# Performance work log

Hardware: AMD Instinct MI355X
Metric: run time of the kernel (lower is better)

## Reference

```python
import jax, jax.numpy as jnp
import numpy as np
from jax import lax

BASE_SIZE = 16.0
FEAT_STRIDE = 16
RATIOS = (0.5, 1.0, 2.0)
SCALES = (8.0, 16.0, 32.0)
N_PRE_NMS = 6000   # eval-mode ProposalCreator defaults
N_POST_NMS = 300
NMS_THRESH = 0.7
MIN_SIZE = 16.0
SCALE = 1.0


def anchor_base():
    # generate_anchor_base: loops ratio-major, scale-minor -> 9 anchors (y1,x1,y2,x2)
    r = jnp.asarray(RATIOS, jnp.float32)
    s = jnp.asarray(SCALES, jnp.float32)
    h = (BASE_SIZE * s[None, :] * jnp.sqrt(r)[:, None]).reshape(-1)
    w = (BASE_SIZE * s[None, :] * jnp.sqrt(1.0 / r)[:, None]).reshape(-1)
    c = BASE_SIZE / 2.0
    return jnp.stack([c - h / 2, c - w / 2, c + h / 2, c + w / 2], axis=1)  # [9,4]


def enumerate_anchors(hh, ww):
    # replicates _enumerate_shift_anchor incl. torch.meshgrid(shift_x, shift_y) 'ij' ordering
    sy = jnp.arange(hh, dtype=jnp.float32) * FEAT_STRIDE
    sx = jnp.arange(ww, dtype=jnp.float32) * FEAT_STRIDE
    gx, gy = jnp.meshgrid(sx, sy, indexing='ij')  # shapes [ww, hh]
    shift = jnp.stack([gy.ravel(), gx.ravel(), gy.ravel(), gx.ravel()], axis=1)  # [K,4]
    a = anchor_base()[None, :, :] + shift[:, None, :]  # [K,9,4]
    return a.reshape(-1, 4)


def conv2d(x, w, b, pad):
    y = lax.conv_general_dilated(x, w, (1, 1), [(pad, pad), (pad, pad)],
                                 dimension_numbers=('NCHW', 'OIHW', 'NCHW'))
    return y + b[None, :, None, None]


def loc2bbox(anchor, loc):
    h = anchor[:, 2] - anchor[:, 0]
    w = anchor[:, 3] - anchor[:, 1]
    cy = anchor[:, 0] + 0.5 * h
    cx = anchor[:, 1] + 0.5 * w
    dy, dx, dh, dw = loc[:, 0], loc[:, 1], loc[:, 2], loc[:, 3]
    cy = dy * h + cy
    cx = dx * w + cx
    h = jnp.exp(dh) * h
    w = jnp.exp(dw) * w
    return jnp.stack([cy - 0.5 * h, cx - 0.5 * w, cy + 0.5 * h, cx + 0.5 * w], axis=1)


def propose(loc, score, anchor, img_h, img_w):
    # ProposalCreator for a single image: decode, clip, min-size filter, top-k, NMS, pad to N_POST_NMS
    roi = loc2bbox(anchor, loc)
    roi = jnp.stack([jnp.clip(roi[:, 0], 0.0, img_h), jnp.clip(roi[:, 1], 0.0, img_w),
                     jnp.clip(roi[:, 2], 0.0, img_h), jnp.clip(roi[:, 3], 0.0, img_w)], axis=1)
    ms = MIN_SIZE * SCALE
    valid = ((roi[:, 2] - roi[:, 0]) >= ms) & ((roi[:, 3] - roi[:, 1]) >= ms)
    score = jnp.where(valid, score, -jnp.inf)
    top_s, order = lax.top_k(score, N_PRE_NMS)          # score-descending candidates
    boxes = roi[order]                                   # [N_PRE,4]
    valid_s = top_s > -jnp.inf
    # pairwise IoU [N_PRE,N_PRE]
    area = (boxes[:, 2] - boxes[:, 0]) * (boxes[:, 3] - boxes[:, 1])
    tl = jnp.maximum(boxes[:, None, :2], boxes[None, :, :2])
    br = jnp.minimum(boxes[:, None, 2:], boxes[None, :, 2:])
    inter = jnp.prod(jnp.clip(br - tl, 0.0, None), axis=-1)
    iou = lax.stop_gradient(inter / (area[:, None] + area[None, :] - inter))
    idxs = jnp.arange(N_PRE_NMS)
    def body(keep, i):
        sup = (iou[i] > NMS_THRESH) & (idxs > i) & keep[i]
        return keep & ~sup, None
    keep, _ = lax.scan(body, valid_s, idxs)              # greedy NMS over score-sorted boxes
    # kept indices in score order (stable argsort: True(kept) sorts first as 0)
    sel = jnp.argsort(jnp.logical_not(keep))[:N_POST_NMS]
    out_valid = jnp.arange(N_POST_NMS) < jnp.sum(keep)
    return jnp.where(out_valid[:, None], boxes[sel], 0.0)  # [N_POST,4], zero-padded


def rpn_forward(x, conv1_w, conv1_b, score_w, score_b, loc_w, loc_b, img_h, img_w):
    n, _, hh, ww = x.shape
    anchor = enumerate_anchors(hh, ww)                   # [hh*ww*9, 4]
    A = anchor.shape[0] // (hh * ww)
    feat = jax.nn.relu(conv2d(x, conv1_w, conv1_b, 1))   # [n,512,hh,ww]
    locs = conv2d(feat, loc_w, loc_b, 0).transpose(0, 2, 3, 1).reshape(n, -1, 4)
    raw_scores = conv2d(feat, score_w, score_b, 0).transpose(0, 2, 3, 1)  # [n,hh,ww,A*2]
    fg = jax.nn.softmax(raw_scores.reshape(n, hh, ww, A, 2), axis=4)[..., 1].reshape(n, -1)
    scores = raw_scores.reshape(n, -1, 2)
    rois = jax.vmap(lambda l, s: propose(l, s, anchor, float(img_h), float(img_w)))(locs, fg)
    roi_indices = jnp.broadcast_to(jnp.arange(n, dtype=jnp.int32)[:, None], (n, N_POST_NMS))
    return locs, scores, rois, roi_indices, anchor


def setup_inputs() -> dict:
    key = jax.random.key(0)
    ks = jax.random.split(key, 4)
    x = jax.random.normal(ks[0], (4, 512, 50, 50), jnp.float32)
    conv1_w = jax.random.normal(ks[1], (512, 512, 3, 3), jnp.float32) * 0.01
    conv1_b = jnp.zeros((512,), jnp.float32)
    score_w = jax.random.normal(ks[2], (18, 512, 1, 1), jnp.float32) * 0.01
    score_b = jnp.zeros((18,), jnp.float32)
    loc_w = jax.random.normal(ks[3], (36, 512, 1, 1), jnp.float32) * 0.01
    loc_b = jnp.zeros((36,), jnp.float32)
    return {'x': x, 'conv1_w': conv1_w, 'conv1_b': conv1_b, 'score_w': score_w,
            'score_b': score_b, 'loc_w': loc_w, 'loc_b': loc_b, 'img_h': 800, 'img_w': 800}


def reference(x, conv1_w, conv1_b, score_w, score_b, loc_w, loc_b, img_h, img_w):
    return rpn_forward(x, conv1_w, conv1_b, score_w, score_b, loc_w, loc_b, img_h, img_w)
```

## Files before the change

kernel.cpp:

```cpp
#include <hip/hip_runtime.h>
#include <stdint.h>

#define NB 4
#define CIN 512
#define PIX 2500
#define KTOT 4608
#define NBOX 22500
#define NPRE 6000
#define NPOST 300
#define NWORD 94
#define SCAP 8192

#define O_LOCS   0
#define O_SCORES 360000
#define O_ROIS   540000
#define O_RIDX   544800
#define O_ANCH   546000

#define XT_ROWS 2960
#define XT_FRONT 64
#define XT_IMG (XT_ROWS * 512)
#define XT_SPLIT_BYTES ((size_t)NB * XT_IMG * 2)

#define WO_XT1   0ull
#define WO_XT2   12124160ull
#define WO_WSBLK 24248320ull
#define WO_FEATP 33685504ull
#define WO_WT    74645504ull
#define WO_BOXES 74760192ull
#define WO_DKEY  76200192ull
#define WO_BOX6K 76560192ull
#define WO_VALID 76944192ull
#define WO_MASK  0ull

#define FEATP_HALF 5120000

typedef _Float16 h8 __attribute__((ext_vector_type(8)));
typedef float f32x4 __attribute__((ext_vector_type(4)));
typedef unsigned int u32;
typedef unsigned long long u64;

__device__ __forceinline__ void gll16(const void* g, void* l) {
  __builtin_amdgcn_global_load_lds((const __attribute__((address_space(1))) u32*)g,
                                   (__attribute__((address_space(3))) u32*)l, 16, 0, 0);
}

__device__ __forceinline__ float rd_dim(const int* p) {
  int v = *p;
  if (v > 0 && v < 1000000) return (float)v;
  return __int_as_float(v);
}

__global__ void k_zero(u32* __restrict__ xt) {
  size_t n = (2 * XT_SPLIT_BYTES) / 4;
  for (size_t i = blockIdx.x * 256ull + threadIdx.x; i < n; i += (size_t)gridDim.x * 256)
    xt[i] = 0u;
}

__global__ void k_xT(const float* __restrict__ x, _Float16* __restrict__ x1,
                     _Float16* __restrict__ x2) {
  __shared__ float sx[3200];
  int chunk = blockIdx.x, r0 = blockIdx.y, b = blockIdx.z;
  int t = threadIdx.x;
  int ic0 = chunk * 64;
  for (int i = t; i < 3200; i += 256) {
    int icl = i / 50, c = i - icl * 50;
    sx[i] = x[(((size_t)b * 512 + ic0 + icl) * 50 + r0) * 50 + c];
  }
  __syncthreads();
  for (int j = t; j < 3200; j += 256) {
    int c = j >> 6, icl = j & 63;
    float v = sx[icl * 50 + c];
    _Float16 h1 = (_Float16)v;
    _Float16 h2 = (_Float16)(v - (float)h1);
    size_t dst = (size_t)b * XT_IMG + (size_t)(XT_FRONT + (r0 + 1) * 52 + (c + 1)) * 512 + ic0 + icl;
    x1[dst] = h1;
    x2[dst] = h2;
  }
}

__global__ void k_splitw(const float* __restrict__ w, _Float16* __restrict__ wblk) {
  int n = 4 * 144 * 16 * 512;
  for (int idx = blockIdx.x * 256 + threadIdx.x; idx < n; idx += gridDim.x * 256) {
    int lane8 = idx & 511;
    int l = lane8 >> 3, j = lane8 & 7;
    int reg = (idx >> 9) & 15;
    int t = idx >> 13;
    int ksI = t % 144, mt = t / 144;
    int ocs = reg >> 1, s = reg & 1;
    int oc = mt * 128 + ocs * 16 + (l & 15);
    int k = ksI * 32 + (l >> 4) * 8 + j;
    int tap = k >> 9, ic = k & 511;
    float v = w[((size_t)oc * 512 + ic) * 9 + tap];
    _Float16 h1 = (_Float16)v;
    wblk[idx] = s ? (_Float16)(v - (float)h1) : h1;
  }
}

__global__ void k_wt(const float* __restrict__ loc_w, const float* __restrict__ score_w,
                     float* __restrict__ wt) {
  int idx = blockIdx.x * 256 + threadIdx.x;
  if (idx >= 128 * 56 * 4) return;
  int i = idx & 3, j = (idx >> 2) % 56, c4 = idx / 224;
  int c = c4 * 4 + i;
  float v = 0.f;
  if (j < 36) v = loc_w[(size_t)j * 512 + c];
  else if (j < 54) v = score_w[(size_t)(j - 36) * 512 + c];
  wt[idx] = v;
}

__global__ __launch_bounds__(128, 2) void k_conv(
    const _Float16* __restrict__ xs1, const _Float16* __restrict__ xs2,
    const _Float16* __restrict__ wsBlk,
    float* __restrict__ featP) {
  __shared__ _Float16 lds[16384];
  int id = blockIdx.x;
  int bz = id & 7;
  int inner = id >> 3;
  int st = inner / 44;
  int idx2 = inner - st * 44;
  int nt = idx2 >> 1;
  int mt = st * 2 + (idx2 & 1);
  int b = bz >> 1, ks = bz & 1;
  int t = threadIdx.x, lane = t & 63, w = t >> 6;
  int mb = mt * 128, nb = nt * 128;
  int l15 = lane & 15, l4 = lane >> 4;
  const _Float16* xi1 = xs1 + (size_t)b * XT_IMG + (size_t)XT_FRONT * 512;
  const _Float16* xi2 = xs2 + (size_t)b * XT_IMG + (size_t)XT_FRONT * 512;
  const _Float16* wbase = wsBlk + ((size_t)(mt * 144 + ks * 72) * 16 + w * 8) * 512 + lane * 8;

  f32x4 acc[4][8];
#pragma unroll
  for (int i = 0; i < 4; i++)
#pragma unroll
    for (int j = 0; j < 8; j++)
      acc[i][j] = (f32x4){0.f, 0.f, 0.f, 0.f};

  auto stageB = [&](int kk, int off) {
    int kg = ks * 2304 + kk * 32;
    int tap = kg >> 9, ic0 = kg & 511;
    int sh = (tap / 3 - 1) * 52 + (tap % 3) - 1;
#pragma unroll
    for (int u = 0; u < 8; u++) {
      int r = w * 8 + u;
      int pxs = r >> 1, s = r & 1;
      const _Float16* xp = s ? xi2 : xi1;
      int qp = nb + pxs * 16 + l15 + sh;
      gll16(xp + (ptrdiff_t)qp * 512 + ic0 + l4 * 8, &lds[off + r * 512]);
    }
  };
  auto loadA = [&](int kk, h8* a) {
    const _Float16* p = wbase + (size_t)kk * 16 * 512;
#pragma unroll
    for (int u = 0; u < 8; u++) a[u] = *(const h8*)(p + u * 512);
  };
  auto compute = [&](int off, const h8* a) {
#pragma unroll
    for (int nf = 0; nf < 8; nf++) {
      h8 b0 = *(const h8*)&lds[off + (nf * 2 + 0) * 512 + lane * 8];
      h8 b1 = *(const h8*)&lds[off + (nf * 2 + 1) * 512 + lane * 8];
      __builtin_amdgcn_s_setprio(1);
#pragma unroll
      for (int mf = 0; mf < 4; mf++) {
        acc[mf][nf] = __builtin_amdgcn_mfma_f32_16x16x32_f16(a[mf * 2 + 0], b0, acc[mf][nf], 0, 0, 0);
        acc[mf][nf] = __builtin_amdgcn_mfma_f32_16x16x32_f16(a[mf * 2 + 0], b1, acc[mf][nf], 0, 0, 0);
        acc[mf][nf] = __builtin_amdgcn_mfma_f32_16x16x32_f16(a[mf * 2 + 1], b0, acc[mf][nf], 0, 0, 0);
      }
      __builtin_amdgcn_s_setprio(0);
    }
  };

  h8 aA[8], aB[8];
  loadA(0, aA);
  stageB(0, 0);
  __syncthreads();
#pragma unroll 1
  for (int kp = 0; kp < 36; kp++) {
    int kk = 2 * kp;
    stageB(kk + 1, 8192);
    loadA(kk + 1, aB);
    compute(0, aA);
    __syncthreads();
    if (kp < 35) {
      stageB(kk + 2, 0);
      loadA(kk + 2, aA);
    }
    compute(8192, aB);
    __syncthreads();
  }

  float* fp = featP + (size_t)ks * FEATP_HALF;
#pragma unroll
  for (int nf = 0; nf < 8; nf++) {
    int q = nb + nf * 16 + l15;
    int r = q / 52, c = q - r * 52;
    if (r >= 1 && r <= 50 && c >= 1 && c <= 50) {
      int p = (r - 1) * 50 + (c - 1);
      size_t base = ((size_t)b * PIX + p) * 512;
#pragma unroll
      for (int mf = 0; mf < 4; mf++) {
        int oc0 = mb + w * 64 + mf * 16 + l4 * 4;
        *(float4*)&fp[base + oc0] = make_float4(acc[mf][nf][0], acc[mf][nf][1],
                                                acc[mf][nf][2], acc[mf][nf][3]);
      }
    }
  }
}

__global__ __launch_bounds__(256) void k_heads(const float* __restrict__ featP,
                                               const float* __restrict__ wt4,
                                               const float* __restrict__ conv_b,
                                               const float* __restrict__ loc_b,
                                               const float* __restrict__ score_b,
                                               const int* __restrict__ ihp,
                                               const int* __restrict__ iwp,
                                               float* __restrict__ out,
                                               float* __restrict__ boxes,
                                               uint32_t* __restrict__ dkey) {
  int wid = blockIdx.x * 4 + (threadIdx.x >> 6);
  if (wid >= NB * PIX) return;
  int lane = threadIdx.x & 63;
  int b = wid / PIX, p = wid % PIX;
  int row = lane < 54 ? lane : 54;
  const float* f0 = featP + ((size_t)b * PIX + p) * 512;
  const float* f1 = f0 + FEATP_HALF;
  float acc = 0.f;
  for (int c4 = 0; c4 < 128; c4++) {
    float4 u = *(const float4*)(f0 + c4 * 4);
    float4 v = *(const float4*)(f1 + c4 * 4);
    float4 bb = *(const float4*)(conv_b + c4 * 4);
    float4 wv = *(const float4*)(wt4 + ((size_t)c4 * 56 + row) * 4);
    acc += fmaxf(u.x + v.x + bb.x, 0.f) * wv.x;
    acc += fmaxf(u.y + v.y + bb.y, 0.f) * wv.y;
    acc += fmaxf(u.z + v.z + bb.z, 0.f) * wv.z;
    acc += fmaxf(u.w + v.w + bb.w, 0.f) * wv.w;
  }
  float bi = 0.f;
  if (lane < 36) bi = loc_b[lane];
  else if (lane < 54) bi = score_b[lane - 36];
  acc += bi;
  if (lane < 36) out[O_LOCS + (size_t)b * 90000 + (size_t)p * 36 + lane] = acc;
  else if (lane < 54) out[O_SCORES + (size_t)b * 45000 + (size_t)p * 18 + (lane - 36)] = acc;

  float imgH = rd_dim(ihp), imgW = rd_dim(iwp);
  int gy = p % 50, gx = p / 50;
  float sy = 16.f * gy, sx = 16.f * gx;

  int a9 = (lane < 9) ? lane : 0;
  float dy  = __shfl(acc, a9 * 4 + 0);
  float dxv = __shfl(acc, a9 * 4 + 1);
  float dh  = __shfl(acc, a9 * 4 + 2);
  float dw  = __shfl(acc, a9 * 4 + 3);
  float l0  = __shfl(acc, 36 + a9 * 2);
  float l1  = __shfl(acc, 36 + a9 * 2 + 1);

  {
    float rr = (a9 < 3) ? 0.5f : (a9 < 6 ? 1.f : 2.f);
    int si = a9 % 3;
    float ssc = (si == 0) ? 8.f : (si == 1 ? 16.f : 32.f);
    float hb = 16.f * ssc * sqrtf(rr);
    float wb = 16.f * ssc * sqrtf(1.f / rr);
    float ay1 = (8.f - hb * 0.5f) + sy;
    float ax1 = (8.f - wb * 0.5f) + sx;
    float ay2 = (8.f + hb * 0.5f) + sy;
    float ax2 = (8.f + wb * 0.5f) + sx;
    float h = ay2 - ay1, w2d = ax2 - ax1;
    float cy = ay1 + 0.5f * h, cx = ax1 + 0.5f * w2d;
    float cy2 = dy * h + cy, cx2 = dxv * w2d + cx;
    float h2 = expf(dh) * h, ww2 = expf(dw) * w2d;
    float y1 = cy2 - 0.5f * h2, x1 = cx2 - 0.5f * ww2;
    float y2 = cy2 + 0.5f * h2, x2 = cx2 + 0.5f * ww2;
    y1 = fminf(fmaxf(y1, 0.f), imgH);
    x1 = fminf(fmaxf(x1, 0.f), imgW);
    y2 = fminf(fmaxf(y2, 0.f), imgH);
    x2 = fminf(fmaxf(x2, 0.f), imgW);
    bool valid = (y2 - y1 >= 16.f) && (x2 - x1 >= 16.f);
    float m = fmaxf(l0, l1);
    float e0 = expf(l0 - m), e1 = expf(l1 - m);
    float fg = e1 / (e0 + e1);
    float scv = valid ? fg : -INFINITY;
    if (lane < 9) {
      size_t k = (size_t)b * NBOX + (size_t)p * 9 + a9;
      *(float4*)(boxes + k * 4) = make_float4(y1, x1, y2, x2);
      uint32_t u = __float_as_uint(scv);
      uint32_t f2 = (u >> 31) ? ~u : (u | 0x80000000u);
      dkey[k] = ~f2;
    }
  }
  if (b == 0 && lane < 36) {
    int aa = lane >> 2, dd = lane & 3;
    float rr2 = (aa < 3) ? 0.5f : (aa < 6 ? 1.f : 2.f);
    int si2 = aa % 3;
    float ss2 = (si2 == 0) ? 8.f : (si2 == 1 ? 16.f : 32.f);
    float hb2 = 16.f * ss2 * sqrtf(rr2);
    float wb2 = 16.f * ss2 * sqrtf(1.f / rr2);
    float v;
    if (dd == 0) v = (8.f - hb2 * 0.5f) + sy;
    else if (dd == 1) v = (8.f - wb2 * 0.5f) + sx;
    else if (dd == 2) v = (8.f + hb2 * 0.5f) + sy;
    else v = (8.f + wb2 * 0.5f) + sx;
    out[O_ANCH + (size_t)p * 36 + lane] = v;
  }
}

__global__ void k_topk(const uint32_t* __restrict__ dkey, const float* __restrict__ boxes,
                       float* __restrict__ box6k,
                       unsigned long long* __restrict__ validm) {
  extern __shared__ char smem[];
  u64* cand = (u64*)smem;
  u64* alt  = (u64*)(smem + 65536);
  u32* hcnt = (u32*)(smem + 131072);
  u32* wc     = (u32*)(smem + 139264);
  u32* digTot = wc + 16;
  u32* digBase = digTot + 16;
  u32* msc = digBase + 16;
  u32* histw = (u32*)(smem + 65536);
  u32* hist = histw + 4096;
  int b = blockIdx.x, tid = threadIdx.x;
  int wq = tid >> 6, l = tid & 63;
  const uint32_t* dk = dkey + (size_t)b * NBOX;

  uint32_t P = 0, need = NPRE;
  for (int pass = 0; pass < 4; pass++) {
    int sh = 24 - 8 * pass;
    for (int i = tid; i < 16 * 256; i += 1024) histw[i] = 0;
    __syncthreads();
    for (int i = tid; i < NBOX; i += 1024) {
      uint32_t d = dk[i];
      bool match = (((uint64_t)d >> (sh + 8)) == ((uint64_t)P >> (sh + 8)));
      if (match) atomicAdd(&histw[wq * 256 + ((d >> sh) & 255u)], 1u);
    }
    __syncthreads();
    for (int bin = tid; bin < 256; bin += 1024) {
      uint32_t s = 0;
#pragma unroll
      for (int q = 0; q < 16; q++) s += histw[q * 256 + bin];
      hist[bin] = s;
    }
    __syncthreads();
    if (tid == 0) {
      uint32_t cum = 0, v = 0;
      for (; v < 255; v++) {
        if (cum + hist[v] >= need) break;
        cum += hist[v];
      }
      msc[0] = v;
      msc[1] = cum;
    }
    __syncthreads();
    need -= msc[1];
    P |= msc[0] << sh;
    __syncthreads();
  }
  uint32_t Dstar = P;

  if (tid == 0) msc[2] = 0;
  __syncthreads();
  for (int c = 0; c < 22; c++) {
    int i = c * 1024 + tid;
    uint32_t d = (i < NBOX) ? dk[i] : 0xFFFFFFFFu;
    bool pred = (i < NBOX) && (d <= Dstar);
    u64 bal = __ballot(pred);
    uint32_t rank = (uint32_t)__popcll(bal & ((1ull << l) - 1ull));
    __syncthreads();
    if (l == 0) wc[wq] = (uint32_t)__popcll(bal);
    __syncthreads();
    if (tid == 0) {
      uint32_t run = msc[2];
      for (int q = 0; q < 16; q++) { uint32_t v = wc[q]; wc[q] = run; run += v; }
      msc[2] = run;
    }
    __syncthreads();
    if (pred) {
      uint32_t pos = wc[wq] + rank;
      if (pos < SCAP) cand[pos] = ((u64)d << 32) | (uint32_t)i;
    }
  }
  __syncthreads();
  uint32_t cnt = msc[2] < SCAP ? msc[2] : SCAP;
  for (int i = (int)cnt + tid; i < SCAP; i += 1024) cand[i] = ~0ull;
  __syncthreads();

  u64* src = cand;
  u64* dst = alt;
  for (int pass = 0; pass < 8; pass++) {
    int sh = 32 + pass * 4;
    for (int i = tid; i < 2048; i += 1024) hcnt[i] = 0;
    __syncthreads();
    for (int c = 0; c < 8; c++) {
      int i = c * 1024 + tid;
      uint32_t dig = (uint32_t)(src[i] >> sh) & 15u;
      u64 m = ~0ull;
#pragma unroll
      for (int bit = 0; bit < 4; bit++) {
        u64 bb = __ballot((dig >> bit) & 1u);
        m &= ((dig >> bit) & 1u) ? bb : ~bb;
      }
      if (l == __builtin_ctzll(m)) hcnt[(i >> 6) * 16 + dig] = (uint32_t)__popcll(m);
    }
    __syncthreads();
    if (tid < 16) {
      uint32_t run = 0;
      for (int u = 0; u < 128; u++) {
        uint32_t v = hcnt[u * 16 + tid];
        hcnt[u * 16 + tid] = run;
        run += v;
      }
      digTot[tid] = run;
    }
    __syncthreads();
    if (tid == 0) {
      uint32_t basev = 0;
      for (int d2 = 0; d2 < 16; d2++) { digBase[d2] = basev; basev += digTot[d2]; }
    }
    __syncthreads();
    for (int c = 0; c < 8; c++) {
      int i = c * 1024 + tid;
      u64 key = src[i];
      uint32_t dig = (uint32_t)(key >> sh) & 15u;
      u64 m = ~0ull;
#pragma unroll
      for (int bit = 0; bit < 4; bit++) {
        u64 bb = __ballot((dig >> bit) & 1u);
        m &= ((dig >> bit) & 1u) ? bb : ~bb;
      }
      uint32_t rank = (uint32_t)__popcll(m & ((1ull << l) - 1ull));
      uint32_t dpos = digBase[dig] + hcnt[(i >> 6) * 16 + dig] + rank;
      dst[dpos] = key;
    }
    __syncthreads();
    u64* tmp = src; src = dst; dst = tmp;
  }

  for (int r = tid; r < NPRE; r += 1024) {
    u64 kk = cand[r];
    uint32_t idx = (uint32_t)kk;
    float4 bx = *(const float4*)(boxes + ((size_t)b * NBOX + idx) * 4);
    *(float4*)(box6k + ((size_t)b * NPRE + r) * 4) = bx;
  }
  for (int wi = tid; wi < NWORD; wi += 1024) {
    unsigned long long m = 0ull;
    for (int bb = 0; bb < 64; bb++) {
      int r = wi * 64 + bb;
      if (r < NPRE) {
        uint32_t d = (uint32_t)(cand[r] >> 32);
        if (d < 0xFF800000u) m |= (1ull << bb);
      }
    }
    validm[b * NWORD + wi] = m;
  }
}

__global__ __launch_bounds__(256) void k_mask(const float* __restrict__ box6k,
                                              unsigned long long* __restrict__ mask) {
  int b = blockIdx.z, it = blockIdx.x, wt = blockIdx.y;
  int t = threadIdx.x;
  int il = t & 31, wl = t >> 5;
  if (wt * 512 + 511 <= it * 32) return;
  __shared__ float bi[32][4];
  __shared__ float bj[512][4];
  if (t < 128) {
    int ii = it * 32 + (t >> 2);
    if (ii > NPRE - 1) ii = NPRE - 1;
    bi[t >> 2][t & 3] = box6k[((size_t)b * NPRE + ii) * 4 + (t & 3)];
  }
#pragma unroll
  for (int q = 0; q < 2; q++) {
    int v = t + 256 * q;
    int jg = wt * 512 + v;
    float4 f = make_float4(0.f, 0.f, 0.f, 0.f);
    if (jg < NPRE) f = *(const float4*)(box6k + ((size_t)b * NPRE + jg) * 4);
    *(float4*)&bj[v][0] = f;
  }
  __syncthreads();
  int i = it * 32 + il;
  int w = wt * 8 + wl;
  if (i >= NPRE || w >= NWORD) return;
  float y1 = bi[il][0], x1 = bi[il][1], y2 = bi[il][2], x2 = bi[il][3];
  float ar = (y2 - y1) * (x2 - x1);
  unsigned long long m = 0ull;
  int jbase = w * 64;
  for (int jj = 0; jj < 64; jj++) {
    int j = jbase + jj;
    int js = wl * 64 + jj;
    float jy1 = bj[js][0], jx1 = bj[js][1], jy2 = bj[js][2], jx2 = bj[js][3];
    float tlY = fmaxf(y1, jy1), tlX = fmaxf(x1, jx1);
    float brY = fminf(y2, jy2), brX = fminf(x2, jx2);
    float ih = fmaxf(brY - tlY, 0.f), iw2 = fmaxf(brX - tlX, 0.f);
    float inter = ih * iw2;
    float arj = (jy2 - jy1) * (jx2 - jx1);
    float iou = inter / (ar + arj - inter);
    if (iou > 0.7f && j > i && j < NPRE) m |= (1ull << jj);
  }
  mask[((size_t)b * NPRE + i) * NWORD + w] = m;
}

__global__ void k_scan(const unsigned long long* __restrict__ mask,
                       const unsigned long long* __restrict__ validm,
                       const float* __restrict__ box6k, float* __restrict__ out) {
  int b = blockIdx.x;
  int lane = threadIdx.x;
  const unsigned long long* mb = mask + (size_t)b * NPRE * NWORD;
  u64 a0 = (lane < NWORD) ? validm[b * NWORD + lane] : 0ull;
  u64 a1 = (lane + 64 < NWORD) ? validm[b * NWORD + lane + 64] : 0ull;
  __shared__ int keptIdx[NPOST];
  int cnt = 0;
  bool done = false;
  u64 rowCur = mb[(size_t)lane * NWORD + 0];
  for (int w = 0; w < NWORD && !done; w++) {
    u64 rowNext = 0ull;
    if (w + 1 < NWORD) {
      int i2 = (w + 1) * 64 + lane;
      if (i2 < NPRE) rowNext = mb[(size_t)i2 * NWORD + (w + 1)];
    }
    u64 alive = (w < 64) ? __shfl(a0, w) : __shfl(a1, w - 64);
    if (alive) {
      u64 keep = 0ull;
      while (alive) {
        int q = __builtin_ctzll(alive);
        alive &= alive - 1;
        keep |= (1ull << q);
        if (lane == 0) keptIdx[cnt] = w * 64 + q;
        cnt++;
        if (cnt >= NPOST) { done = true; break; }
        alive &= ~__shfl(rowCur, q);
      }
      if (w < 64) { if (lane == w) a0 = 0ull; }
      else        { if (lane == w - 64) a1 = 0ull; }
      if (!done) {
        while (keep) {
          u64 or0 = 0ull, or1 = 0ull;
#pragma unroll
          for (int z = 0; z < 8; z++) {
            if (keep) {
              int q = __builtin_ctzll(keep);
              keep &= keep - 1;
              int ki = w * 64 + q;
              u64 m0 = (lane < NWORD && lane > w) ? mb[(size_t)ki * NWORD + lane] : 0ull;
              u64 m1 = (lane + 64 < NWORD && lane + 64 > w) ? mb[(size_t)ki * NWORD + 64 + lane] : 0ull;
              or0 |= m0;
              or1 |= m1;
            }
          }
          a0 &= ~or0;
          a1 &= ~or1;
        }
      }
    }
    rowCur = rowNext;
  }
  __syncthreads();
  for (int r = lane; r < NPOST; r += 64) {
    float4 bx = make_float4(0.f, 0.f, 0.f, 0.f);
    if (r < cnt) bx = *(const float4*)(box6k + ((size_t)b * NPRE + keptIdx[r]) * 4);
    *(float4*)(out + O_ROIS + ((size_t)b * NPOST + r) * 4) = bx;
    out[O_RIDX + b * NPOST + r] = (float)b;
  }
}

extern "C" void kernel_launch(void* const* d_in, const int* in_sizes, int n_in,
                              void* d_out, int out_size, void* d_ws, size_t ws_size,
                              hipStream_t stream) {
  const float* x       = (const float*)d_in[0];
  const float* conv1_w = (const float*)d_in[1];
  const float* conv1_b = (const float*)d_in[2];
  const float* score_w = (const float*)d_in[3];
  const float* score_b = (const float*)d_in[4];
  const float* loc_w   = (const float*)d_in[5];
  const float* loc_b   = (const float*)d_in[6];
  const int* ihp = (const int*)d_in[7];
  const int* iwp = (const int*)d_in[8];
  float* out = (float*)d_out;
  char* ws = (char*)d_ws;
  _Float16* xt1 = (_Float16*)(ws + WO_XT1);
  _Float16* xt2 = (_Float16*)(ws + WO_XT2);
  _Float16* wsBlk = (_Float16*)(ws + WO_WSBLK);
  float* featP = (float*)(ws + WO_FEATP);
  float* wt    = (float*)(ws + WO_WT);
  float* boxes = (float*)(ws + WO_BOXES);
  uint32_t* dkey  = (uint32_t*)(ws + WO_DKEY);
  float* box6k = (float*)(ws + WO_BOX6K);
  unsigned long long* validm = (unsigned long long*)(ws + WO_VALID);
  unsigned long long* mask   = (unsigned long long*)(ws + WO_MASK);

  k_zero<<<2048, 256, 0, stream>>>((u32*)xt1);
  k_xT<<<dim3(8, 50, NB), 256, 0, stream>>>(x, xt1, xt2);
  k_splitw<<<2048, 256, 0, stream>>>(conv1_w, wsBlk);
  k_wt<<<(128 * 56 * 4 + 255) / 256, 256, 0, stream>>>(loc_w, score_w, wt);
  k_conv<<<704, 128, 0, stream>>>(xt1, xt2, wsBlk, featP);
  k_heads<<<(NB * PIX + 3) / 4, 256, 0, stream>>>(featP, wt, conv1_b, loc_b, score_b,
                                                  ihp, iwp, out, boxes, dkey);
  int topk_lds = 65536 * 2 + 8192 + 512;
  hipFuncSetAttribute((const void*)k_topk, hipFuncAttributeMaxDynamicSharedMemorySize,
                      topk_lds);
  k_topk<<<NB, 1024, topk_lds, stream>>>(dkey, boxes, box6k, validm);
  dim3 gm(188, 12, NB);
  k_mask<<<gm, 256, 0, stream>>>(box6k, mask);
  k_scan<<<NB, 64, 0, stream>>>(mask, validm, box6k, out);
}
```

Baseline: 644.1 us.

## Halve conv N-tile to double grid, parallelize top-k scans with wave shuffles

The conv kernel's pixel tile shrinks from 128 to 64. That halves LDS and accumulator use per block and doubles the grid to 1408 blocks, raising occupancy and CU coverage at the cost of less weight reuse per block. Separately, several serial single-thread prefix scans in the top-k kernel become wave-level shuffle scans: histogram threshold search, per-wave compaction offsets and radix digit offsets. This cuts serialized latency between barriers.

```diff
diff --git a/kernel.cpp b/kernel.cpp
--- a/kernel.cpp
+++ b/kernel.cpp
@@ -113,27 +113,27 @@
     const _Float16* __restrict__ xs1, const _Float16* __restrict__ xs2,
     const _Float16* __restrict__ wsBlk,
     float* __restrict__ featP) {
-  __shared__ _Float16 lds[16384];
+  __shared__ _Float16 lds[8192];
   int id = blockIdx.x;
   int bz = id & 7;
   int inner = id >> 3;
-  int st = inner / 44;
-  int idx2 = inner - st * 44;
+  int st = inner / 88;
+  int idx2 = inner - st * 88;
   int nt = idx2 >> 1;
   int mt = st * 2 + (idx2 & 1);
   int b = bz >> 1, ks = bz & 1;
   int t = threadIdx.x, lane = t & 63, w = t >> 6;
-  int mb = mt * 128, nb = nt * 128;
+  int mb = mt * 128, nb = nt * 64;
   int l15 = lane & 15, l4 = lane >> 4;
   const _Float16* xi1 = xs1 + (size_t)b * XT_IMG + (size_t)XT_FRONT * 512;
   const _Float16* xi2 = xs2 + (size_t)b * XT_IMG + (size_t)XT_FRONT * 512;
   const _Float16* wbase = wsBlk + ((size_t)(mt * 144 + ks * 72) * 16 + w * 8) * 512 + lane * 8;
 
-  f32x4 acc[4][8];
+  f32x4 acc[4][4];
 #pragma unroll
   for (int i = 0; i < 4; i++)
 #pragma unroll
-    for (int j = 0; j < 8; j++)
+    for (int j = 0; j < 4; j++)
       acc[i][j] = (f32x4){0.f, 0.f, 0.f, 0.f};
 
   auto stageB = [&](int kk, int off) {
@@ -141,8 +141,8 @@
     int tap = kg >> 9, ic0 = kg & 511;
     int sh = (tap / 3 - 1) * 52 + (tap % 3) - 1;
 #pragma unroll
-    for (int u = 0; u < 8; u++) {
-      int r = w * 8 + u;
+    for (int u = 0; u < 4; u++) {
+      int r = w * 4 + u;
       int pxs = r >> 1, s = r & 1;
       const _Float16* xp = s ? xi2 : xi1;
       int qp = nb + pxs * 16 + l15 + sh;
@@ -156,7 +156,7 @@
   };
   auto compute = [&](int off, const h8* a) {
 #pragma unroll
-    for (int nf = 0; nf < 8; nf++) {
+    for (int nf = 0; nf < 4; nf++) {
       h8 b0 = *(const h8*)&lds[off + (nf * 2 + 0) * 512 + lane * 8];
       h8 b1 = *(const h8*)&lds[off + (nf * 2 + 1) * 512 + lane * 8];
       __builtin_amdgcn_s_setprio(1);
@@ -177,7 +177,7 @@
 #pragma unroll 1
   for (int kp = 0; kp < 36; kp++) {
     int kk = 2 * kp;
-    stageB(kk + 1, 8192);
+    stageB(kk + 1, 4096);
     loadA(kk + 1, aB);
     compute(0, aA);
     __syncthreads();
@@ -185,13 +185,13 @@
       stageB(kk + 2, 0);
       loadA(kk + 2, aA);
     }
-    compute(8192, aB);
+    compute(4096, aB);
     __syncthreads();
   }
 
   float* fp = featP + (size_t)ks * FEATP_HALF;
 #pragma unroll
-  for (int nf = 0; nf < 8; nf++) {
+  for (int nf = 0; nf < 4; nf++) {
     int q = nb + nf * 16 + l15;
     int r = q / 52, c = q - r * 52;
     if (r >= 1 && r <= 50 && c >= 1 && c <= 50) {
@@ -338,14 +338,31 @@
       hist[bin] = s;
     }
     __syncthreads();
-    if (tid == 0) {
-      uint32_t cum = 0, v = 0;
-      for (; v < 255; v++) {
-        if (cum + hist[v] >= need) break;
-        cum += hist[v];
-      }
-      msc[0] = v;
-      msc[1] = cum;
+    if (tid < 64) {
+      uint32_t h0 = hist[l * 4 + 0], h1 = hist[l * 4 + 1];
+      uint32_t h2 = hist[l * 4 + 2], h3 = hist[l * 4 + 3];
+      uint32_t p1 = h0, p2 = h0 + h1, p3 = p2 + h2, p4 = p3 + h3;
+      uint32_t s = p4;
+#pragma unroll
+      for (int dd = 1; dd < 64; dd <<= 1) { uint32_t v = __shfl_up(s, dd); if (l >= dd) s += v; }
+      uint32_t excl = s - p4;
+      uint32_t i0 = excl + p1, i1 = excl + p2, i2 = excl + p3, i3 = excl + p4;
+      int local = 4;
+      if (i0 >= need) local = 0;
+      else if (i1 >= need) local = 1;
+      else if (i2 >= need) local = 2;
+      else if (i3 >= need) local = 3;
+      u64 bal = __ballot(local < 4);
+      int lw = bal ? __builtin_ctzll(bal) : 63;
+      if (l == lw) {
+        if (local < 4) {
+          msc[0] = (uint32_t)(l * 4 + local);
+          msc[1] = (local == 0) ? excl : (local == 1) ? i0 : (local == 2) ? i1 : i2;
+        } else {
+          msc[0] = 255u;
+          msc[1] = i2;
+        }
+      }
     }
     __syncthreads();
     need -= msc[1];
@@ -365,10 +382,14 @@
     __syncthreads();
     if (l == 0) wc[wq] = (uint32_t)__popcll(bal);
     __syncthreads();
-    if (tid == 0) {
-      uint32_t run = msc[2];
-      for (int q = 0; q < 16; q++) { uint32_t v = wc[q]; wc[q] = run; run += v; }
-      msc[2] = run;
+    if (tid < 64) {
+      uint32_t v = (l < 16) ? wc[l] : 0u;
+      uint32_t s = v;
+#pragma unroll
+      for (int dd = 1; dd < 16; dd <<= 1) { uint32_t t2 = __shfl_up(s, dd); if (l >= dd) s += t2; }
+      uint32_t base0 = msc[2];
+      if (l < 16) wc[l] = base0 + s - v;
+      if (l == 15) msc[2] = base0 + s;
     }
     __syncthreads();
     if (pred) {
@@ -399,14 +420,23 @@
       if (l == __builtin_ctzll(m)) hcnt[(i >> 6) * 16 + dig] = (uint32_t)__popcll(m);
     }
     __syncthreads();
-    if (tid < 16) {
-      uint32_t run = 0;
-      for (int u = 0; u < 128; u++) {
-        uint32_t v = hcnt[u * 16 + tid];
-        hcnt[u * 16 + tid] = run;
-        run += v;
-      }
-      digTot[tid] = run;
+    {
+      int d = wq;
+      uint32_t cl = hcnt[l * 16 + d];
+      uint32_t ch = hcnt[(l + 64) * 16 + d];
+      uint32_t s = cl;
+#pragma unroll
+      for (int dd = 1; dd < 64; dd <<= 1) { uint32_t v = __shfl_up(s, dd); if (l >= dd) s += v; }
+      uint32_t tl = __shfl(s, 63);
+      uint32_t el = s - cl;
+      uint32_t s2 = ch;
+#pragma unroll
+      for (int dd = 1; dd < 64; dd <<= 1) { uint32_t v = __shfl_up(s2, dd); if (l >= dd) s2 += v; }
+      uint32_t th = __shfl(s2, 63);
+      uint32_t eh = tl + (s2 - ch);
+      hcnt[l * 16 + d] = el;
+      hcnt[(l + 64) * 16 + d] = eh;
+      if (l == 0) digTot[d] = tl + th;
     }
     __syncthreads();
     if (tid == 0) {
@@ -587,7 +617,7 @@
   k_xT<<<dim3(8, 50, NB), 256, 0, stream>>>(x, xt1, xt2);
   k_splitw<<<2048, 256, 0, stream>>>(conv1_w, wsBlk);
   k_wt<<<(128 * 56 * 4 + 255) / 256, 256, 0, stream>>>(loc_w, score_w, wt);
-  k_conv<<<704, 128, 0, stream>>>(xt1, xt2, wsBlk, featP);
+  k_conv<<<1408, 128, 0, stream>>>(xt1, xt2, wsBlk, featP);
   k_heads<<<(NB * PIX + 3) / 4, 256, 0, stream>>>(featP, wt, conv1_b, loc_b, score_b,
                                                   ihp, iwp, out, boxes, dkey);
   int topk_lds = 65536 * 2 + 8192 + 512;
```

Result: faster. 607.7 us (-5.7%).
